# Kernel tuning notes

Measured on AMD Instinct MI355X. Metric: run time of the kernel, lower is better.

## Reference

```python
import jax, jax.numpy as jnp
import numpy as np

V, B, L, NG = 50000, 128, 350, 3        # vocab, batch(docs), doc length, n-gram window
D, H, C = 768, 256, 20                  # bert dim, num_hidden, class_num
HEADS, LAYERS, K, ALPHA = 8, 2, 3, 0.15 # GAT heads/layers, diffusion hops k, alpha


def setup_inputs() -> dict:
    rng = np.random.default_rng(0)
    # per-doc graphs: 350 unique word-ids per doc (nodes), n-gram window edges
    node_ids = np.stack([rng.choice(V, L, replace=False) for _ in range(B)]).ravel()
    src_b, dst_b = [], []
    for i in range(L):
        for j in range(max(0, i - NG), min(L, i + NG + 1)):
            src_b.append(i); dst_b.append(j)
    src_b, dst_b = np.asarray(src_b), np.asarray(dst_b)
    off = (np.arange(B) * L)[:, None]
    edge_src = (src_b[None, :] + off).ravel()
    edge_dst = (dst_b[None, :] + off).ravel()
    graph_id = np.repeat(np.arange(B), L)

    ks = jax.random.split(jax.random.key(0), 8)
    f32 = jnp.float32
    return {
        'node_ids': jnp.asarray(node_ids, jnp.int32),
        'edge_src': jnp.asarray(edge_src, jnp.int32),
        'edge_dst': jnp.asarray(edge_dst, jnp.int32),
        'graph_id': jnp.asarray(graph_id, jnp.int32),
        'emb':    (jax.random.normal(ks[0], (V, D), f32) * 0.02),
        'W1':     (jax.random.normal(ks[1], (D, H), f32) / np.sqrt(D)).astype(f32),
        'b1':     jnp.zeros((H,), f32),
        'W2':     (jax.random.normal(ks[2], (H, C), f32) / np.sqrt(H)).astype(f32),
        'b2':     jnp.zeros((C,), f32),
        'gat_W':  (jax.random.normal(ks[3], (LAYERS, HEADS, C, C), f32) / np.sqrt(C)).astype(f32),
        'a_src':  (jax.random.normal(ks[4], (LAYERS, HEADS, C), f32) * 0.1),
        'a_dst':  (jax.random.normal(ks[5], (LAYERS, HEADS, C), f32) * 0.1),
        'w_gate': (jax.random.normal(ks[6], (C,), f32) / np.sqrt(C)).astype(f32),
        'b_gate': jnp.zeros((), f32),
    }


def _gat_layer(h, W, a_s, a_d, src, dst, N):
    # h: [N,C]; W: [Hd,C,C]; a_s/a_d: [Hd,C]
    z = jnp.einsum('nc,hcd->hnd', h, W)                     # [Hd,N,C]
    e = jax.nn.leaky_relu(jnp.einsum('hnd,hd->hn', z, a_s)[:, src]
                          + jnp.einsum('hnd,hd->hn', z, a_d)[:, dst], 0.2)  # [Hd,E]

    def segsoftmax(ev):  # edge softmax over incoming edges at each dst node
        m = jax.ops.segment_max(ev, dst, num_segments=N)
        ex = jnp.exp(ev - m[dst])
        s = jax.ops.segment_sum(ex, dst, num_segments=N)
        return ex / (s[dst] + 1e-9)

    att = jax.vmap(segsoftmax)(e)                           # [Hd,E]

    def diffuse(zh, ah):  # attention diffusion: Z_t = (1-a) A Z_{t-1} + a Z_0
        zt = zh
        for _ in range(K):
            agg = jax.ops.segment_sum(ah[:, None] * zt[src], dst, num_segments=N)
            zt = (1.0 - ALPHA) * agg + ALPHA * zh
        return zt

    out = jax.vmap(diffuse)(z, att)                         # [Hd,N,C]
    return jax.nn.elu(out).mean(axis=0)                     # merge='mean'


def reference(node_ids, edge_src, edge_dst, graph_id, emb, W1, b1, W2, b2,
              gat_W, a_src, a_dst, w_gate, b_gate):
    N = node_ids.shape[0]
    x = emb[node_ids]                                       # [N,768] gather
    x = jax.nn.relu(x @ W1 + b1)                            # linear1 + ReLU
    h = x @ W2 + b2                                         # linear2 -> [N,C]
    for l in range(LAYERS):
        h = _gat_layer(h, gat_W[l], a_src[l], a_dst[l], edge_src, edge_dst, N)
    gate = jax.nn.sigmoid(h @ w_gate + b_gate)[:, None]     # WeightAndSum gate
    return jax.ops.segment_sum(gate * h, graph_id, num_segments=B)  # [B,C]
```

## Files before the change

kernel.cpp:

```cpp
#include <hip/hip_runtime.h>
#include <hip/hip_bf16.h>
#include <cstddef>

#define NB_NODES 44800
#define NDOCS 128
#define DLEN 350
#define DIM 768
#define HID 256
#define NCLS 20
#define NHEADS 8
#define ZROW 352

typedef __bf16 v8bf __attribute__((ext_vector_type(8)));
typedef __bf16 v4bf __attribute__((ext_vector_type(4)));
typedef __bf16 v2bf __attribute__((ext_vector_type(2)));
typedef float v4f __attribute__((ext_vector_type(4)));
typedef float v2f __attribute__((ext_vector_type(2)));

__global__ __launch_bounds__(256) void k_transpose(const float* __restrict__ W1,
                                                   __bf16* __restrict__ W1T) {
  int idx = blockIdx.x * 256 + threadIdx.x;
  int n = idx / 768, k = idx - n * 768;
  W1T[idx] = (__bf16)W1[k * 256 + n];
}

__global__ __launch_bounds__(256) void k_mlp(
    const int* __restrict__ node_ids, const float* __restrict__ emb,
    const __bf16* __restrict__ W1T, const float* __restrict__ b1,
    const float* __restrict__ W2, const float* __restrict__ b2,
    float* __restrict__ h0) {
  __shared__ __align__(16) char smem[26880];
  __bf16* As = (__bf16*)smem;
  float*  xs = (float*)smem;
  __bf16* w2s = (__bf16*)(smem + 16640);
  int tid = threadIdx.x;
  int wave = tid >> 6, lane = tid & 63;
  int quad = lane >> 4, l16 = lane & 15;
  int m0 = blockIdx.x * 32;

  int lrow = tid & 15;
  int lk4  = (tid >> 4) & 3;
  int khalf = (tid >> 6) & 1;
  int msubA = tid >> 7;
  int kbase = khalf * 32 + lk4 * 8;
  const float* ap = emb + (size_t)node_ids[m0 + msubA * 16 + lrow] * DIM + kbase;

  v4f acc[2][4];
#pragma unroll
  for (int ms = 0; ms < 2; ++ms)
#pragma unroll
    for (int j = 0; j < 4; ++j) acc[ms][j] = (v4f){0.f, 0.f, 0.f, 0.f};

  v4f pf0 = *(const v4f*)(ap), pf1 = *(const v4f*)(ap + 4);

  for (int kc = 0; kc < 12; ++kc) {
    __bf16* buf = As + (kc & 1) * 2048;
    v8bf w0;
#pragma unroll
    for (int e = 0; e < 4; ++e) {
      w0[e] = (__bf16)pf0[e]; w0[4 + e] = (__bf16)pf1[e];
    }
    *(v8bf*)(buf + tid * 8) = w0;
    if (kc < 11) {
      int k1 = (kc + 1) * 64;
      pf0 = *(const v4f*)(ap + k1); pf1 = *(const v4f*)(ap + k1 + 4);
    }
    __syncthreads();

#pragma unroll
    for (int ks = 0; ks < 2; ++ks) {
      v8bf af[2], bv[4];
#pragma unroll
      for (int ms = 0; ms < 2; ++ms)
        af[ms] = *(const v8bf*)(buf + ((ms * 2 + ks) * 64 + lane) * 8);
#pragma unroll
      for (int j = 0; j < 4; ++j)
        bv[j] = *(const v8bf*)(W1T + (size_t)(wave * 64 + j * 16 + l16) * DIM + kc * 64 + ks * 32 + quad * 8);
#pragma unroll
      for (int ms = 0; ms < 2; ++ms)
#pragma unroll
        for (int j = 0; j < 4; ++j)
          acc[ms][j] = __builtin_amdgcn_mfma_f32_16x16x32_bf16(af[ms], bv[j], acc[ms][j], 0, 0, 0);
    }
  }

  __syncthreads();
  for (int i = tid; i < HID * NCLS; i += 256) w2s[i] = (__bf16)W2[i];

#pragma unroll
  for (int ms = 0; ms < 2; ++ms) {
    __syncthreads();
#pragma unroll
    for (int j = 0; j < 4; ++j) {
      int col = wave * 64 + j * 16 + l16;
      float bb = b1[col];
#pragma unroll
      for (int r = 0; r < 4; ++r) {
        int lr = quad * 4 + r;
        float v = acc[ms][j][r] + bb;
        xs[lr * 260 + col] = v > 0.f ? v : 0.f;
      }
    }
    __syncthreads();
    if (tid < 160) {
      int m = tid / 10, c0 = (tid % 10) * 2;
      float s0 = b2[c0], s1 = b2[c0 + 1];
      for (int k = 0; k < HID; ++k) {
        float x = xs[m * 260 + k];
        v2bf w = *(const v2bf*)(w2s + k * NCLS + c0);
        s0 += x * (float)w[0]; s1 += x * (float)w[1];
      }
      v2f o; o[0] = s0; o[1] = s1;
      *(v2f*)(h0 + (size_t)(m0 + ms * 16 + m) * NCLS + c0) = o;
    }
  }
}

__global__ __launch_bounds__(384) void k_gat(
    const float* __restrict__ hin, const float* __restrict__ gatW,
    const float* __restrict__ a_src, const float* __restrict__ a_dst,
    int layer, float* __restrict__ zout) {
  __shared__ float zT[NCLS * ZROW];
  __shared__ float asv[DLEN], adv[DLEN];
  int tid = threadIdx.x;
  int head = blockIdx.x & 7;
  int doc = blockIdx.x >> 3;
  const float* W  = gatW  + (size_t)(layer * NHEADS + head) * NCLS * NCLS;
  const float* av = a_src + (layer * NHEADS + head) * NCLS;
  const float* dv = a_dst + (layer * NHEADS + head) * NCLS;
  int r = tid;
  bool act = r < DLEN;

  float z0[NCLS];
  if (act) {
    const float* hr = hin + ((size_t)doc * DLEN + r) * NCLS;
    float h[NCLS];
#pragma unroll
    for (int q = 0; q < 5; ++q) {
      v4f t = *(const v4f*)(hr + q * 4);
#pragma unroll
      for (int e = 0; e < 4; ++e) h[q * 4 + e] = t[e];
    }
    float zacc[NCLS];
#pragma unroll
    for (int d = 0; d < NCLS; ++d) zacc[d] = 0.f;
#pragma unroll
    for (int c = 0; c < NCLS; ++c) {
      float hc = h[c];
#pragma unroll
      for (int d = 0; d < NCLS; ++d) zacc[d] += hc * W[c * NCLS + d];
    }
    float sa = 0.f, sd = 0.f;
#pragma unroll
    for (int d = 0; d < NCLS; ++d) { sa += zacc[d] * av[d]; sd += zacc[d] * dv[d]; }
    asv[r] = sa; adv[r] = sd;
#pragma unroll
    for (int c = 0; c < NCLS; ++c) zT[c * ZROW + r] = zacc[c];
#pragma unroll
    for (int d = 0; d < NCLS; ++d) z0[d] = zacc[d];
  }
  __syncthreads();

  float att[7];
  if (act) {
    float ad = adv[r];
    float e[7]; float m = -1e30f;
#pragma unroll
    for (int j = 0; j < 7; ++j) {
      int s = r - 3 + j;
      bool valid = (s >= 0) && (s < DLEN);
      float x = valid ? asv[s] + ad : -1e30f;
      x = x > 0.f ? x : 0.2f * x;
      e[j] = valid ? x : -1e30f;
      if (e[j] > m) m = e[j];
    }
    float sum = 0.f;
#pragma unroll
    for (int j = 0; j < 7; ++j) {
      float ex = (e[j] > -1e29f) ? expf(e[j] - m) : 0.f;
      e[j] = ex; sum += ex;
    }
    float inv = 1.f / (sum + 1e-9f);
#pragma unroll
    for (int j = 0; j < 7; ++j) att[j] = e[j] * inv;
  }

  float vn[NCLS];
  for (int hop = 0; hop < 3; ++hop) {
    if (act) {
      float agg[NCLS];
#pragma unroll
      for (int c = 0; c < NCLS; ++c) agg[c] = 0.f;
#pragma unroll
      for (int j = 0; j < 7; ++j) {
        int s = r - 3 + j;
        s = s < 0 ? 0 : (s > DLEN - 1 ? DLEN - 1 : s);
        float a = att[j];
#pragma unroll
        for (int c = 0; c < NCLS; ++c) agg[c] += a * zT[c * ZROW + s];
      }
#pragma unroll
      for (int c = 0; c < NCLS; ++c) vn[c] = 0.85f * agg[c] + 0.15f * z0[c];
    }
    if (hop < 2) {
      __syncthreads();
      if (act) {
#pragma unroll
        for (int c = 0; c < NCLS; ++c) zT[c * ZROW + r] = vn[c];
      }
      __syncthreads();
    }
  }

  if (act) {
    float* og = zout + ((size_t)head * NB_NODES + (size_t)doc * DLEN + r) * NCLS;
#pragma unroll
    for (int q = 0; q < 5; ++q) {
      v4f t;
#pragma unroll
      for (int e = 0; e < 4; ++e) {
        float x = vn[q * 4 + e];
        t[e] = x > 0.f ? x : expf(x) - 1.f;
      }
      *(v4f*)(og + q * 4) = t;
    }
  }
}

__global__ __launch_bounds__(256) void k_headmean(
    const float* __restrict__ eluzt, float* __restrict__ hout) {
  int idx = blockIdx.x * 256 + threadIdx.x;
  v4f s = (v4f){0.f, 0.f, 0.f, 0.f};
#pragma unroll
  for (int h = 0; h < NHEADS; ++h)
    s += ((const v4f*)eluzt)[(size_t)h * (NB_NODES * NCLS / 4) + idx];
  v4f o; o[0] = s[0] * 0.125f; o[1] = s[1] * 0.125f; o[2] = s[2] * 0.125f; o[3] = s[3] * 0.125f;
  ((v4f*)hout)[idx] = o;
}

__global__ __launch_bounds__(384) void k_hm_pool(
    const float* __restrict__ eluzt, const float* __restrict__ w_gate,
    const float* __restrict__ b_gate, float* __restrict__ out) {
  __shared__ float red[6][NCLS];
  int tid = threadIdx.x;
  int doc = blockIdx.x;
  int r = tid;
  bool act = r < DLEN;

  float wg[NCLS];
#pragma unroll
  for (int c = 0; c < NCLS; ++c) wg[c] = w_gate[c];
  float contrib[NCLS];
#pragma unroll
  for (int c = 0; c < NCLS; ++c) contrib[c] = 0.f;
  if (act) {
    float hm[NCLS];
#pragma unroll
    for (int c = 0; c < NCLS; ++c) hm[c] = 0.f;
#pragma unroll
    for (int hd = 0; hd < NHEADS; ++hd) {
      const float* p = eluzt + ((size_t)hd * NB_NODES + (size_t)doc * DLEN + r) * NCLS;
#pragma unroll
      for (int q = 0; q < 5; ++q) {
        v4f t = *(const v4f*)(p + q * 4);
#pragma unroll
        for (int e = 0; e < 4; ++e) hm[q * 4 + e] += t[e];
      }
    }
    float d = b_gate[0];
#pragma unroll
    for (int c = 0; c < NCLS; ++c) { hm[c] *= 0.125f; d += hm[c] * wg[c]; }
    float g = 1.f / (1.f + expf(-d));
#pragma unroll
    for (int c = 0; c < NCLS; ++c) contrib[c] = g * hm[c];
  }
#pragma unroll
  for (int off = 32; off > 0; off >>= 1)
#pragma unroll
    for (int c = 0; c < NCLS; ++c) contrib[c] += __shfl_down(contrib[c], off);
  int wave = tid >> 6, lane = tid & 63;
  if (lane == 0)
#pragma unroll
    for (int c = 0; c < NCLS; ++c) red[wave][c] = contrib[c];
  __syncthreads();
  if (tid < NCLS) {
    float s = 0.f;
#pragma unroll
    for (int w = 0; w < 6; ++w) s += red[w][tid];
    out[doc * NCLS + tid] = s;
  }
}

extern "C" void kernel_launch(void* const* d_in, const int* in_sizes, int n_in,
                              void* d_out, int out_size, void* d_ws, size_t ws_size,
                              hipStream_t stream) {
  const int* node_ids = (const int*)d_in[0];
  const float* emb    = (const float*)d_in[4];
  const float* W1     = (const float*)d_in[5];
  const float* b1     = (const float*)d_in[6];
  const float* W2     = (const float*)d_in[7];
  const float* b2     = (const float*)d_in[8];
  const float* gatW   = (const float*)d_in[9];
  const float* a_src  = (const float*)d_in[10];
  const float* a_dst  = (const float*)d_in[11];
  const float* w_gate = (const float*)d_in[12];
  const float* b_gate = (const float*)d_in[13];
  float* out = (float*)d_out;
  char* ws = (char*)d_ws;

  __bf16* W1T = (__bf16*)(ws + 0);
  float* hA  = (float*)(ws + 393216);
  float* hB  = (float*)(ws + 3977216);
  float* zt  = (float*)(ws + 7561216);

  k_transpose<<<768, 256, 0, stream>>>(W1, W1T);
  k_mlp<<<NB_NODES / 32, 256, 0, stream>>>(node_ids, emb, W1T, b1, W2, b2, hA);
  k_gat<<<NDOCS * NHEADS, 384, 0, stream>>>(hA, gatW, a_src, a_dst, 0, zt);
  k_headmean<<<(NB_NODES * NCLS / 4) / 256, 256, 0, stream>>>(zt, hB);
  k_gat<<<NDOCS * NHEADS, 384, 0, stream>>>(hB, gatW, a_src, a_dst, 1, zt);
  k_hm_pool<<<NDOCS, 384, 0, stream>>>(zt, w_gate, b_gate, out);
}
```

Measured before the change: 380.1 us.

## Load MFMA A fragments directly from global, drop LDS staging and barriers

The first-layer MLP GEMM used to stage gathered embedding rows into a double-buffered LDS tile, with a __syncthreads each k-chunk. Now each wave loads its own A fragments straight from global memory in the MFMA operand layout, converts them to bf16 in registers, and skips LDS and the per-iteration barriers. The W2 staging also moves to kernel start, which lets the first epilogue barrier go. The cost is redundant global reads: all 4 waves now load the same A rows, where before they shared one LDS copy, and there is no explicit software prefetch any more.

```diff
diff --git a/kernel.cpp b/kernel.cpp
--- a/kernel.cpp
+++ b/kernel.cpp
@@ -30,7 +30,6 @@
     const float* __restrict__ W2, const float* __restrict__ b2,
     float* __restrict__ h0) {
   __shared__ __align__(16) char smem[26880];
-  __bf16* As = (__bf16*)smem;
   float*  xs = (float*)smem;
   __bf16* w2s = (__bf16*)(smem + 16640);
   int tid = threadIdx.x;
@@ -38,12 +37,10 @@
   int quad = lane >> 4, l16 = lane & 15;
   int m0 = blockIdx.x * 32;
 
-  int lrow = tid & 15;
-  int lk4  = (tid >> 4) & 3;
-  int khalf = (tid >> 6) & 1;
-  int msubA = tid >> 7;
-  int kbase = khalf * 32 + lk4 * 8;
-  const float* ap = emb + (size_t)node_ids[m0 + msubA * 16 + lrow] * DIM + kbase;
+  for (int i = tid; i < HID * NCLS; i += 256) w2s[i] = (__bf16)W2[i];
+
+  const float* rp0 = emb + (size_t)node_ids[m0 + l16] * DIM + quad * 8;
+  const float* rp1 = emb + (size_t)node_ids[m0 + 16 + l16] * DIM + quad * 8;
 
   v4f acc[2][4];
 #pragma unroll
@@ -51,45 +48,38 @@
 #pragma unroll
     for (int j = 0; j < 4; ++j) acc[ms][j] = (v4f){0.f, 0.f, 0.f, 0.f};
 
-  v4f pf0 = *(const v4f*)(ap), pf1 = *(const v4f*)(ap + 4);
-
+#pragma unroll 3
   for (int kc = 0; kc < 12; ++kc) {
-    __bf16* buf = As + (kc & 1) * 2048;
-    v8bf w0;
-#pragma unroll
-    for (int e = 0; e < 4; ++e) {
-      w0[e] = (__bf16)pf0[e]; w0[4 + e] = (__bf16)pf1[e];
-    }
-    *(v8bf*)(buf + tid * 8) = w0;
-    if (kc < 11) {
-      int k1 = (kc + 1) * 64;
-      pf0 = *(const v4f*)(ap + k1); pf1 = *(const v4f*)(ap + k1 + 4);
-    }
-    __syncthreads();
-
+    int kb = kc * 64;
 #pragma unroll
     for (int ks = 0; ks < 2; ++ks) {
-      v8bf af[2], bv[4];
-#pragma unroll
-      for (int ms = 0; ms < 2; ++ms)
-        af[ms] = *(const v8bf*)(buf + ((ms * 2 + ks) * 64 + lane) * 8);
+      int ko = kb + ks * 32;
+      v4f a0l = *(const v4f*)(rp0 + ko);
+      v4f a0h = *(const v4f*)(rp0 + ko + 4);
+      v4f a1l = *(const v4f*)(rp1 + ko);
+      v4f a1h = *(const v4f*)(rp1 + ko + 4);
+      v8bf bv[4];
 #pragma unroll
       for (int j = 0; j < 4; ++j)
-        bv[j] = *(const v8bf*)(W1T + (size_t)(wave * 64 + j * 16 + l16) * DIM + kc * 64 + ks * 32 + quad * 8);
-#pragma unroll
-      for (int ms = 0; ms < 2; ++ms)
-#pragma unroll
-        for (int j = 0; j < 4; ++j)
-          acc[ms][j] = __builtin_amdgcn_mfma_f32_16x16x32_bf16(af[ms], bv[j], acc[ms][j], 0, 0, 0);
-    }
-  }
-
-  __syncthreads();
-  for (int i = tid; i < HID * NCLS; i += 256) w2s[i] = (__bf16)W2[i];
+        bv[j] = *(const v8bf*)(W1T + (size_t)(wave * 64 + j * 16 + l16) * DIM + ko + quad * 8);
+      v8bf af0, af1;
+#pragma unroll
+      for (int e = 0; e < 4; ++e) {
+        af0[e] = (__bf16)a0l[e]; af0[4 + e] = (__bf16)a0h[e];
+        af1[e] = (__bf16)a1l[e]; af1[4 + e] = (__bf16)a1h[e];
+      }
+#pragma unroll
+      for (int j = 0; j < 4; ++j)
+        acc[0][j] = __builtin_amdgcn_mfma_f32_16x16x32_bf16(af0, bv[j], acc[0][j], 0, 0, 0);
+#pragma unroll
+      for (int j = 0; j < 4; ++j)
+        acc[1][j] = __builtin_amdgcn_mfma_f32_16x16x32_bf16(af1, bv[j], acc[1][j], 0, 0, 0);
+    }
+  }
 
 #pragma unroll
   for (int ms = 0; ms < 2; ++ms) {
-    __syncthreads();
+    if (ms) __syncthreads();
 #pragma unroll
     for (int j = 0; j < 4; ++j) {
       int col = wave * 64 + j * 16 + l16;
```

Result: slower. 421.9 us (+11.0%).
